# Kernel optimization log

Measured on AMD Instinct MI355X. Metric: run time of the kernel, lower is better.

## Reference

```python
import jax, jax.numpy as jnp
import numpy as np

D = 1024
H = 16
DK = D // H


def setup_inputs() -> dict:
    key = jax.random.key(0)
    ks = jax.random.split(key, 10)
    B, S = 2, 2048
    scale = 1.0 / np.sqrt(D)
    inp = {
        "x": jax.random.normal(ks[0], (B, S, D), dtype=jnp.float32),
        "mask": jax.random.randint(ks[1], (B, S), 0, 2, dtype=jnp.int32),
        "wq": jax.random.normal(ks[2], (D, D), dtype=jnp.float32) * scale,
        "bq": jnp.zeros((D,), dtype=jnp.float32),
        "wk": jax.random.normal(ks[3], (D, D), dtype=jnp.float32) * scale,
        "bk": jnp.zeros((D,), dtype=jnp.float32),
        "wv": jax.random.normal(ks[4], (D, D), dtype=jnp.float32) * scale,
        "bv": jnp.zeros((D,), dtype=jnp.float32),
        "wo": jax.random.normal(ks[5], (D, D), dtype=jnp.float32) * scale,
        "bo": jnp.zeros((D,), dtype=jnp.float32),
    }
    return inp


def reference(x, mask, wq, bq, wk, bk, wv, bv, wo, bo):
    B, S, _ = x.shape
    # torch Linear: y = x @ W.T + b
    def proj(w, b):
        return (jnp.einsum("bsd,ed->bse", x, w) + b).reshape(B, S, H, DK).transpose(0, 2, 1, 3)  # (B,H,S,dk)

    q = proj(wq, bq)
    k = proj(wk, bk)
    v = proj(wv, bv)

    scores = jnp.einsum("bhqd,bhkd->bhqk", q, k) / jnp.sqrt(jnp.float32(DK))  # (B,H,S,S)
    # original: mask.unsqueeze(1).unsqueeze(3) -> (B,1,S,1), masks along the QUERY axis
    m = mask[:, None, :, None]  # (B,1,S,1)
    scores = jnp.where(m == 0, jnp.float32(-1e9), scores)
    attn = jax.nn.softmax(scores, axis=-1)
    ctx = jnp.einsum("bhqk,bhkd->bhqd", attn, v)  # (B,H,S,dk)
    concat = ctx.transpose(0, 2, 1, 3).reshape(B, S, D)
    return jnp.einsum("bsd,ed->bse", concat, wo) + bo
```

## Files before the change

### kernel.cpp

```cpp
#include <hip/hip_runtime.h>
#include <hip/hip_bf16.h>

#define SEQ 2048
#define DM  1024

typedef __attribute__((ext_vector_type(8))) _Float16 f16x8;
typedef __attribute__((ext_vector_type(4)))  float   f32x4;

#define EXP2F(x) __builtin_amdgcn_exp2f(x)

__device__ __forceinline__ ushort f2h(float x) {
    union { _Float16 h; ushort u; } c; c.h = (_Float16)x; return c.u;
}
__device__ __forceinline__ unsigned pk2h(float a, float b) {
    typedef __fp16 fp16v2 __attribute__((ext_vector_type(2)));
    union { fp16v2 h; unsigned u; } c;
    c.h = __builtin_amdgcn_cvt_pkrtz(a, b);
    return c.u;
}

__device__ __forceinline__ void gload16(const void* g, void* l) {
    __builtin_amdgcn_global_load_lds(
        (const __attribute__((address_space(1))) unsigned*)(uintptr_t)g,
        (__attribute__((address_space(3))) unsigned*)(uintptr_t)l, 16, 0, 0);
}

__global__ __launch_bounds__(256)
void cvt_all(const float* __restrict__ x,  const float* __restrict__ wq,
             const float* __restrict__ wk, const float* __restrict__ wv,
             const float* __restrict__ wo,
             ushort* __restrict__ xH, ushort* __restrict__ wH)
{
    const int NX4 = (2 * SEQ * DM) / 4;
    const int NW4 = (DM * DM) / 4;
    const int total = NX4 + 4 * NW4;
    for (int i = blockIdx.x * 256 + threadIdx.x; i < total; i += gridDim.x * 256) {
        float4 v; ushort4* dst;
        if (i < NX4) {
            v = ((const float4*)x)[i];
            dst = (ushort4*)xH + i;
        } else {
            const int j = i - NX4;
            const int wi = j >> 18;
            const int jo = j & (NW4 - 1);
            const float* ws_ = (wi == 0) ? wq : (wi == 1) ? wk : (wi == 2) ? wv : wo;
            v = ((const float4*)ws_)[jo];
            dst = (ushort4*)wH + j;
        }
        ushort4 h;
        h.x = f2h(v.x); h.y = f2h(v.y); h.z = f2h(v.z); h.w = f2h(v.w);
        *dst = h;
    }
}

template<int BM, int BN, int WM, int WN, int MODE>
__global__ __launch_bounds__(WM * WN * 64)
void gemm5(const ushort* __restrict__ A, const ushort* __restrict__ B,
           const float* __restrict__ b0, const float* __restrict__ b1,
           const float* __restrict__ b2,
           ushort* __restrict__ QH, ushort* __restrict__ KH,
           ushort* __restrict__ VH, float* __restrict__ outf, int nmt)
{
    constexpr int NW  = WM * WN;
    constexpr int PR  = BM / WM, PC = BN / WN;
    constexpr int MR  = PR / 16, NR = PC / 16, MH = MR / 2;
    constexpr int APW = (BM / 8) / NW;
    constexpr int BPW = (BN / 8) / NW;
    constexpr int NT  = DM / 64;

    __shared__ ushort A_lds[2][BM * 64];
    __shared__ ushort B_lds[2][BN * 64];

    const int tid = threadIdx.x, w = tid >> 6, lane = tid & 63;
    const int nwg = gridDim.x, q8 = nwg >> 3;
    const int wg  = (blockIdx.x & 7) * q8 + (blockIdx.x >> 3);
    const int m0  = (wg % nmt) * BM, n0 = (wg / nmt) * BN;
    const int wm  = w / WN, wn = w % WN;

    auto stage = [&](int buf, int kt) {
        const int k0 = kt * 64;
#pragma unroll
        for (int j = 0; j < APW; ++j) {
            const int s   = w * APW + j;
            const int row = s * 8 + (lane >> 3);
            const int cl  = (lane & 7) ^ (row & 7);
            gload16(A + (size_t)(m0 + row) * DM + k0 + cl * 8,
                    &A_lds[buf][s * 512]);
        }
#pragma unroll
        for (int j = 0; j < BPW; ++j) {
            const int s   = w * BPW + j;
            const int row = s * 8 + (lane >> 3);
            const int cl  = (lane & 7) ^ (row & 7);
            gload16(B + (size_t)(n0 + row) * DM + k0 + cl * 8,
                    &B_lds[buf][s * 512]);
        }
    };

    f32x4 acc[MR][NR];
#pragma unroll
    for (int i = 0; i < MR; ++i)
#pragma unroll
        for (int j = 0; j < NR; ++j) acc[i][j] = f32x4{0.f, 0.f, 0.f, 0.f};

    stage(0, 0);
    stage(1, 1);

    for (int t = 0; t < NT; ++t) {
        const int buf = t & 1;
        if (t == NT - 1) asm volatile("s_waitcnt vmcnt(0)" ::: "memory");
        else             asm volatile("s_waitcnt vmcnt(8)" ::: "memory");
        __builtin_amdgcn_sched_barrier(0);
        __builtin_amdgcn_s_barrier();

        f16x8 bf_[NR][2];
#pragma unroll
        for (int nf = 0; nf < NR; ++nf) {
            const int r = wn * PC + nf * 16 + (lane & 15);
#pragma unroll
            for (int kb = 0; kb < 2; ++kb) {
                const int c = kb * 4 + (lane >> 4);
                bf_[nf][kb] = *(const f16x8*)&B_lds[buf][r * 64 + ((c ^ (r & 7)) << 3)];
            }
        }
#pragma unroll
        for (int qm = 0; qm < 2; ++qm) {
            f16x8 af_[MH][2];
#pragma unroll
            for (int mf = 0; mf < MH; ++mf) {
                const int r = wm * PR + qm * (PR / 2) + mf * 16 + (lane & 15);
#pragma unroll
                for (int kb = 0; kb < 2; ++kb) {
                    const int c = kb * 4 + (lane >> 4);
                    af_[mf][kb] = *(const f16x8*)&A_lds[buf][r * 64 + ((c ^ (r & 7)) << 3)];
                }
            }
            __builtin_amdgcn_s_setprio(1);
#pragma unroll
            for (int kb = 0; kb < 2; ++kb)
#pragma unroll
                for (int mf = 0; mf < MH; ++mf)
#pragma unroll
                    for (int nf = 0; nf < NR; ++nf)
                        acc[qm * MH + mf][nf] = __builtin_amdgcn_mfma_f32_16x16x32_f16(
                            af_[mf][kb], bf_[nf][kb], acc[qm * MH + mf][nf], 0, 0, 0);
            __builtin_amdgcn_s_setprio(0);
        }
        __builtin_amdgcn_sched_barrier(0);
        __builtin_amdgcn_s_barrier();
        __builtin_amdgcn_sched_barrier(0);
        if (t + 2 < NT) stage(buf, t + 2);
    }

#pragma unroll
    for (int mf = 0; mf < MR; ++mf)
#pragma unroll
        for (int nf = 0; nf < NR; ++nf) {
            const int col  = n0 + wn * PC + nf * 16 + (lane & 15);
            const int row0 = m0 + wm * PR + mf * 16 + ((lane >> 4) << 2);
            f32x4 v = acc[mf][nf];
            if constexpr (MODE == 1) {
                float4 o;
                o.x = v[0] + b0[row0 + 0];
                o.y = v[1] + b0[row0 + 1];
                o.z = v[2] + b0[row0 + 2];
                o.w = v[3] + b0[row0 + 3];
                *(float4*)&outf[(size_t)col * DM + row0] = o;
            } else {
                const int sel = row0 >> 10;
                const int e = row0 & 1023;
                const int b = col >> 11, s = col & 2047;
                const int h = e >> 6, dk = e & 63;
                const float* bp = (sel == 0) ? b0 : (sel == 1) ? b1 : b2;
                const float sc = (sel == 0) ? 0.125f * 1.44269504089f : 1.0f;
                const float v0 = (v[0] + bp[e + 0]) * sc;
                const float v1 = (v[1] + bp[e + 1]) * sc;
                const float v2 = (v[2] + bp[e + 2]) * sc;
                const float v3 = (v[3] + bp[e + 3]) * sc;
                const int bh = b * 16 + h;
                ushort4 hv;
                hv.x = f2h(v0); hv.y = f2h(v1); hv.z = f2h(v2); hv.w = f2h(v3);
                if (sel == 0) {
                    const size_t off = ((size_t)bh * SEQ + s) * 64 + dk;
                    *(ushort4*)&QH[off] = hv;
                } else if (sel == 1) {
                    const size_t off = ((size_t)bh * SEQ + s) * 64 + dk;
                    *(ushort4*)&KH[off] = hv;
                } else {
                    const size_t o0 = ((size_t)bh * 64 + dk) * SEQ + s;
                    VH[o0]           = hv.x;
                    VH[o0 + SEQ]     = hv.y;
                    VH[o0 + 2 * SEQ] = hv.z;
                    VH[o0 + 3 * SEQ] = hv.w;
                }
            }
        }
}

__global__ __launch_bounds__(512, 2)
void attn_k(const ushort* __restrict__ QH, const ushort* __restrict__ KH,
            const ushort* __restrict__ VH, const int* __restrict__ mask,
            ushort* __restrict__ ch)
{
    __shared__ ushort Ks[2][64 * 64];
    __shared__ ushort Vs[2][64 * 64];
    __shared__ ushort Ps[8][16 * 64];

    const int t = threadIdx.x, w = t >> 6, lane = t & 63;
    const int wg = (blockIdx.x & 7) * 64 + (blockIdx.x >> 3);
    const int bh = wg >> 4, qt = wg & 15;
    const int b = bh >> 4, h = bh & 15;
    const int q0 = qt * 128 + w * 16;
    const size_t base = (size_t)bh * SEQ * 64;
    const int lq = lane & 15, cb = lane >> 4;

    const int msk = mask[b * SEQ + q0 + lq];
    f16x8 qf[2];
#pragma unroll
    for (int kb = 0; kb < 2; ++kb) {
        qf[kb] = *(const f16x8*)&QH[base + (size_t)(q0 + lq) * 64 + kb * 32 + cb * 8];
        if (msk == 0) qf[kb] = f16x8{0, 0, 0, 0, 0, 0, 0, 0};
    }

    float m_run = -1e30f, l_run = 0.f;
    f32x4 acc[4];
#pragma unroll
    for (int df = 0; df < 4; ++df) acc[df] = f32x4{0.f, 0.f, 0.f, 0.f};

    f16x8 sK, sV;
    const int sr = t >> 3, scc = t & 7;
    const int wr_off = sr * 64 + (scc ^ (sr & 7)) * 8;
    const f16x8* pK = (const f16x8*)&KH[base + (size_t)sr * 64 + scc * 8];
    const ushort* gK = &KH[base + (size_t)sr * 64 + scc * 8];
    const ushort* gV = &VH[base + (size_t)sr * SEQ + scc * 8];
    auto stage_load = [&]() {
        sK = *(const f16x8*)gK;
        sV = *(const f16x8*)gV;
        gK += 64 * 64;
        gV += 64;
    };

    stage_load();
    *(f16x8*)&Ks[0][wr_off] = sK;
    *(f16x8*)&Vs[0][wr_off] = sV;
    stage_load();
    __syncthreads();

    auto body = [&](const int BUF, const bool WR, const bool LD) {
        if (WR) {
            *(f16x8*)&Ks[BUF ^ 1][wr_off] = sK;
            *(f16x8*)&Vs[BUF ^ 1][wr_off] = sV;
        }
        if (LD) stage_load();

        f32x4 st[4];
#pragma unroll
        for (int mf = 0; mf < 4; ++mf) st[mf] = f32x4{0.f, 0.f, 0.f, 0.f};
        __builtin_amdgcn_s_setprio(1);
#pragma unroll
        for (int mf = 0; mf < 4; ++mf) {
            const int r = mf * 16 + lq;
#pragma unroll
            for (int kb = 0; kb < 2; ++kb) {
                const int p = (kb * 4 + cb) ^ (r & 7);
                f16x8 kf = *(const f16x8*)&Ks[BUF][r * 64 + p * 8];
                st[mf] = __builtin_amdgcn_mfma_f32_16x16x32_f16(kf, qf[kb], st[mf], 0, 0, 0);
            }
        }
        __builtin_amdgcn_s_setprio(0);

        {
            float mx = -1e30f;
#pragma unroll
            for (int mf = 0; mf < 4; ++mf)
#pragma unroll
                for (int r4 = 0; r4 < 4; ++r4) mx = fmaxf(mx, st[mf][r4]);
            if (!__all(mx - m_run <= 8.0f)) {
                mx = fmaxf(mx, __shfl_xor(mx, 16));
                mx = fmaxf(mx, __shfl_xor(mx, 32));
                const float mnew = fmaxf(m_run, mx);
                const float corr = EXP2F(m_run - mnew);
                m_run = mnew;
                l_run *= corr;
#pragma unroll
                for (int df = 0; df < 4; ++df)
#pragma unroll
                    for (int r4 = 0; r4 < 4; ++r4) acc[df][r4] *= corr;
            }
            float ss = 0.f;
#pragma unroll
            for (int mf = 0; mf < 4; ++mf)
#pragma unroll
                for (int r4 = 0; r4 < 4; ++r4) {
                    const float p = EXP2F(st[mf][r4] - m_run);
                    st[mf][r4] = p; ss += p;
                }
            ss += __shfl_xor(ss, 16);
            ss += __shfl_xor(ss, 32);
            l_run += ss;
        }

#pragma unroll
        for (int mf = 0; mf < 4; ++mf) {
            const int key0 = mf * 16 + (cb << 2);
            uint2 pw;
            pw.x = pk2h(st[mf][0], st[mf][1]);
            pw.y = pk2h(st[mf][2], st[mf][3]);
            const int p = (key0 >> 3) ^ (lq & 7);
            *(uint2*)&Ps[w][lq * 64 + p * 8 + (key0 & 7)] = pw;
        }

        f16x8 pf[2];
#pragma unroll
        for (int kb = 0; kb < 2; ++kb) {
            const int p = (kb * 4 + cb) ^ (lq & 7);
            pf[kb] = *(const f16x8*)&Ps[w][lq * 64 + p * 8];
        }
        __builtin_amdgcn_s_setprio(1);
#pragma unroll
        for (int df = 0; df < 4; ++df) {
            const int r = df * 16 + lq;
#pragma unroll
            for (int kb = 0; kb < 2; ++kb) {
                const int p = (kb * 4 + cb) ^ (r & 7);
                f16x8 vf = *(const f16x8*)&Vs[BUF][r * 64 + p * 8];
                acc[df] = __builtin_amdgcn_mfma_f32_16x16x32_f16(vf, pf[kb], acc[df], 0, 0, 0);
            }
        }
        __builtin_amdgcn_s_setprio(0);

        __syncthreads();
    };

#pragma unroll 1
    for (int i = 0; i < 15; ++i) {
        body(0, true, true);
        body(1, true, true);
    }
    body(0, true, false);
    body(1, false, false);

    {
        const float inv = 1.0f / l_run;
        const int s = q0 + lq;
#pragma unroll
        for (int df = 0; df < 4; ++df) {
            const int e0 = h * 64 + df * 16 + (cb << 2);
            ushort4 hv;
            hv.x = f2h(acc[df][0] * inv);
            hv.y = f2h(acc[df][1] * inv);
            hv.z = f2h(acc[df][2] * inv);
            hv.w = f2h(acc[df][3] * inv);
            *(ushort4*)&ch[(size_t)(b * SEQ + s) * DM + e0] = hv;
        }
    }
}

extern "C" void kernel_launch(void* const* d_in, const int* in_sizes, int n_in,
                              void* d_out, int out_size, void* d_ws, size_t ws_size,
                              hipStream_t stream)
{
    const float* x  = (const float*)d_in[0];
    const int* mask = (const int*)d_in[1];
    const float* wq = (const float*)d_in[2];
    const float* bq = (const float*)d_in[3];
    const float* wk = (const float*)d_in[4];
    const float* bk = (const float*)d_in[5];
    const float* wv = (const float*)d_in[6];
    const float* bv = (const float*)d_in[7];
    const float* wo = (const float*)d_in[8];
    const float* bo = (const float*)d_in[9];
    float* out = (float*)d_out;

    const size_t M1 = 1024 * 1024;
    ushort* W = (ushort*)d_ws;
    ushort* xH = W;
    ushort* wH = W + 4 * M1;
    ushort* QH = W + 8 * M1;
    ushort* KH = W + 12 * M1;
    ushort* VH = W + 16 * M1;

    cvt_all<<<2048, 256, 0, stream>>>(x, wq, wk, wv, wo, xH, wH);

    gemm5<384, 128, 4, 2, 0><<<256, 512, 0, stream>>>(
        wH, xH, bq, bk, bv, QH, KH, VH, nullptr, 8);

    attn_k<<<512, 512, 0, stream>>>(QH, KH, VH, mask, xH);

    gemm5<128, 128, 2, 2, 1><<<256, 256, 0, stream>>>(
        wH + 3 * M1, xH, bo, nullptr, nullptr,
        nullptr, nullptr, nullptr, out, 8);
}
```

Baseline: 109.9 us.

## Software-pipeline QK^T of the next tile with softmax/PV of the previous tile

Moves the attention kernel to a triple-buffered K/V shared-memory ring. The QK^T MFMAs for tile i+1 are issued before the softmax and PV MFMAs for tile i, so the exp and scalar softmax work can overlap matrix-core work. This costs 8 more score registers per thread and more LDS, which risks spills or lower occupancy. The prefetch also reads one tile past the end of each head.

After: 107.7 us. No clear change (-2.0%).

```diff
diff --git a/kernel.cpp b/kernel.cpp
--- a/kernel.cpp
+++ b/kernel.cpp
@@ -202,8 +202,8 @@
             const ushort* __restrict__ VH, const int* __restrict__ mask,
             ushort* __restrict__ ch)
 {
-    __shared__ ushort Ks[2][64 * 64];
-    __shared__ ushort Vs[2][64 * 64];
+    __shared__ ushort K3[3][64 * 64];
+    __shared__ ushort V3[3][64 * 64];
     __shared__ ushort Ps[8][16 * 64];
 
     const int t = threadIdx.x, w = t >> 6, lane = t & 63;
@@ -227,118 +227,132 @@
 #pragma unroll
     for (int df = 0; df < 4; ++df) acc[df] = f32x4{0.f, 0.f, 0.f, 0.f};
 
+    f32x4 stb[2][4];
+
     f16x8 sK, sV;
     const int sr = t >> 3, scc = t & 7;
     const int wr_off = sr * 64 + (scc ^ (sr & 7)) * 8;
-    const f16x8* pK = (const f16x8*)&KH[base + (size_t)sr * 64 + scc * 8];
     const ushort* gK = &KH[base + (size_t)sr * 64 + scc * 8];
     const ushort* gV = &VH[base + (size_t)sr * SEQ + scc * 8];
-    auto stage_load = [&]() {
-        sK = *(const f16x8*)gK;
-        sV = *(const f16x8*)gV;
-        gK += 64 * 64;
-        gV += 64;
-    };
-
-    stage_load();
-    *(f16x8*)&Ks[0][wr_off] = sK;
-    *(f16x8*)&Vs[0][wr_off] = sV;
-    stage_load();
+
+    sK = *(const f16x8*)gK; sV = *(const f16x8*)gV; gK += 4096; gV += 64;
+    *(f16x8*)&K3[0][wr_off] = sK; *(f16x8*)&V3[0][wr_off] = sV;
+    sK = *(const f16x8*)gK; sV = *(const f16x8*)gV; gK += 4096; gV += 64;
+    *(f16x8*)&K3[1][wr_off] = sK; *(f16x8*)&V3[1][wr_off] = sV;
+    sK = *(const f16x8*)gK; sV = *(const f16x8*)gV; gK += 4096; gV += 64;
     __syncthreads();
 
-    auto body = [&](const int BUF, const bool WR, const bool LD) {
-        if (WR) {
-            *(f16x8*)&Ks[BUF ^ 1][wr_off] = sK;
-            *(f16x8*)&Vs[BUF ^ 1][wr_off] = sV;
-        }
-        if (LD) stage_load();
-
-        f32x4 st[4];
-#pragma unroll
-        for (int mf = 0; mf < 4; ++mf) st[mf] = f32x4{0.f, 0.f, 0.f, 0.f};
-        __builtin_amdgcn_s_setprio(1);
-#pragma unroll
-        for (int mf = 0; mf < 4; ++mf) {
-            const int r = mf * 16 + lq;
-#pragma unroll
-            for (int kb = 0; kb < 2; ++kb) {
-                const int p = (kb * 4 + cb) ^ (r & 7);
-                f16x8 kf = *(const f16x8*)&Ks[BUF][r * 64 + p * 8];
-                st[mf] = __builtin_amdgcn_mfma_f32_16x16x32_f16(kf, qf[kb], st[mf], 0, 0, 0);
-            }
-        }
-        __builtin_amdgcn_s_setprio(0);
-
-        {
-            float mx = -1e30f;
-#pragma unroll
-            for (int mf = 0; mf < 4; ++mf)
-#pragma unroll
-                for (int r4 = 0; r4 < 4; ++r4) mx = fmaxf(mx, st[mf][r4]);
-            if (!__all(mx - m_run <= 8.0f)) {
-                mx = fmaxf(mx, __shfl_xor(mx, 16));
-                mx = fmaxf(mx, __shfl_xor(mx, 32));
-                const float mnew = fmaxf(m_run, mx);
-                const float corr = EXP2F(m_run - mnew);
-                m_run = mnew;
-                l_run *= corr;
-#pragma unroll
-                for (int df = 0; df < 4; ++df)
-#pragma unroll
-                    for (int r4 = 0; r4 < 4; ++r4) acc[df][r4] *= corr;
-            }
-            float ss = 0.f;
-#pragma unroll
-            for (int mf = 0; mf < 4; ++mf)
-#pragma unroll
-                for (int r4 = 0; r4 < 4; ++r4) {
-                    const float p = EXP2F(st[mf][r4] - m_run);
-                    st[mf][r4] = p; ss += p;
-                }
-            ss += __shfl_xor(ss, 16);
-            ss += __shfl_xor(ss, 32);
-            l_run += ss;
-        }
-
-#pragma unroll
-        for (int mf = 0; mf < 4; ++mf) {
-            const int key0 = mf * 16 + (cb << 2);
-            uint2 pw;
-            pw.x = pk2h(st[mf][0], st[mf][1]);
-            pw.y = pk2h(st[mf][2], st[mf][3]);
-            const int p = (key0 >> 3) ^ (lq & 7);
-            *(uint2*)&Ps[w][lq * 64 + p * 8 + (key0 & 7)] = pw;
-        }
-
-        f16x8 pf[2];
-#pragma unroll
-        for (int kb = 0; kb < 2; ++kb) {
-            const int p = (kb * 4 + cb) ^ (lq & 7);
-            pf[kb] = *(const f16x8*)&Ps[w][lq * 64 + p * 8];
-        }
-        __builtin_amdgcn_s_setprio(1);
-#pragma unroll
-        for (int df = 0; df < 4; ++df) {
-            const int r = df * 16 + lq;
-#pragma unroll
-            for (int kb = 0; kb < 2; ++kb) {
-                const int p = (kb * 4 + cb) ^ (r & 7);
-                f16x8 vf = *(const f16x8*)&Vs[BUF][r * 64 + p * 8];
-                acc[df] = __builtin_amdgcn_mfma_f32_16x16x32_f16(vf, pf[kb], acc[df], 0, 0, 0);
-            }
-        }
-        __builtin_amdgcn_s_setprio(0);
-
-        __syncthreads();
-    };
+#define QKM(B3, CUR)                                                          \
+    {                                                                         \
+        _Pragma("unroll")                                                     \
+        for (int mf = 0; mf < 4; ++mf) stb[CUR][mf] = f32x4{0.f,0.f,0.f,0.f}; \
+        __builtin_amdgcn_s_setprio(1);                                        \
+        _Pragma("unroll")                                                     \
+        for (int mf = 0; mf < 4; ++mf) {                                      \
+            const int r_ = mf * 16 + lq;                                      \
+            _Pragma("unroll")                                                 \
+            for (int kb = 0; kb < 2; ++kb) {                                  \
+                const int p_ = (kb * 4 + cb) ^ (r_ & 7);                      \
+                f16x8 kf = *(const f16x8*)&K3[B3][r_ * 64 + p_ * 8];          \
+                stb[CUR][mf] = __builtin_amdgcn_mfma_f32_16x16x32_f16(        \
+                    kf, qf[kb], stb[CUR][mf], 0, 0, 0);                       \
+            }                                                                 \
+        }                                                                     \
+        __builtin_amdgcn_s_setprio(0);                                        \
+    }
+
+#define FINP(PRV, VB)                                                         \
+    {                                                                         \
+        float ma = fmaxf(fmaxf(stb[PRV][0][0], stb[PRV][0][1]),               \
+                         fmaxf(stb[PRV][0][2], stb[PRV][0][3]));              \
+        float mb = fmaxf(fmaxf(stb[PRV][1][0], stb[PRV][1][1]),               \
+                         fmaxf(stb[PRV][1][2], stb[PRV][1][3]));              \
+        float mc = fmaxf(fmaxf(stb[PRV][2][0], stb[PRV][2][1]),               \
+                         fmaxf(stb[PRV][2][2], stb[PRV][2][3]));              \
+        float md = fmaxf(fmaxf(stb[PRV][3][0], stb[PRV][3][1]),               \
+                         fmaxf(stb[PRV][3][2], stb[PRV][3][3]));              \
+        float mx = fmaxf(fmaxf(ma, mb), fmaxf(mc, md));                       \
+        if (!__all(mx - m_run <= 8.0f)) {                                     \
+            mx = fmaxf(mx, __shfl_xor(mx, 16));                               \
+            mx = fmaxf(mx, __shfl_xor(mx, 32));                               \
+            const float mnew = fmaxf(m_run, mx);                              \
+            const float corr = EXP2F(m_run - mnew);                           \
+            m_run = mnew;                                                     \
+            l_run *= corr;                                                    \
+            _Pragma("unroll")                                                 \
+            for (int df = 0; df < 4; ++df)                                    \
+                _Pragma("unroll")                                             \
+                for (int r4 = 0; r4 < 4; ++r4) acc[df][r4] *= corr;           \
+        }                                                                     \
+        float parts[4];                                                       \
+        _Pragma("unroll")                                                     \
+        for (int mf = 0; mf < 4; ++mf) {                                      \
+            float e0 = EXP2F(stb[PRV][mf][0] - m_run);                        \
+            float e1 = EXP2F(stb[PRV][mf][1] - m_run);                        \
+            float e2 = EXP2F(stb[PRV][mf][2] - m_run);                        \
+            float e3 = EXP2F(stb[PRV][mf][3] - m_run);                        \
+            parts[mf] = (e0 + e1) + (e2 + e3);                                \
+            uint2 pw;                                                         \
+            pw.x = pk2h(e0, e1);                                              \
+            pw.y = pk2h(e2, e3);                                              \
+            const int key0 = mf * 16 + (cb << 2);                             \
+            const int p_ = (key0 >> 3) ^ (lq & 7);                            \
+            *(uint2*)&Ps[w][lq * 64 + p_ * 8 + (key0 & 7)] = pw;              \
+        }                                                                     \
+        float ss = (parts[0] + parts[1]) + (parts[2] + parts[3]);             \
+        ss += __shfl_xor(ss, 16);                                             \
+        ss += __shfl_xor(ss, 32);                                             \
+        l_run += ss;                                                          \
+        f16x8 pf[2];                                                          \
+        _Pragma("unroll")                                                     \
+        for (int kb = 0; kb < 2; ++kb) {                                      \
+            const int p_ = (kb * 4 + cb) ^ (lq & 7);                          \
+            pf[kb] = *(const f16x8*)&Ps[w][lq * 64 + p_ * 8];                 \
+        }                                                                     \
+        __builtin_amdgcn_s_setprio(1);                                        \
+        _Pragma("unroll")                                                     \
+        for (int df = 0; df < 4; ++df) {                                      \
+            const int r_ = df * 16 + lq;                                      \
+            _Pragma("unroll")                                                 \
+            for (int kb = 0; kb < 2; ++kb) {                                  \
+                const int p_ = (kb * 4 + cb) ^ (r_ & 7);                      \
+                f16x8 vf = *(const f16x8*)&V3[VB][r_ * 64 + p_ * 8];          \
+                acc[df] = __builtin_amdgcn_mfma_f32_16x16x32_f16(             \
+                    vf, pf[kb], acc[df], 0, 0, 0);                            \
+            }                                                                 \
+        }                                                                     \
+        __builtin_amdgcn_s_setprio(0);                                        \
+    }
+
+#define STEP(B3, WB, VB, CUR, PRV)                                            \
+    {                                                                         \
+        QKM(B3, CUR);                                                         \
+        *(f16x8*)&K3[WB][wr_off] = sK;                                        \
+        *(f16x8*)&V3[WB][wr_off] = sV;                                        \
+        sK = *(const f16x8*)gK;                                               \
+        sV = *(const f16x8*)gV;                                               \
+        gK += 4096; gV += 64;                                                 \
+        FINP(PRV, VB);                                                        \
+        __syncthreads();                                                      \
+    }
+
+    QKM(0, 0);
 
 #pragma unroll 1
-    for (int i = 0; i < 15; ++i) {
-        body(0, true, true);
-        body(1, true, true);
-    }
-    body(0, true, false);
-    body(1, false, false);
+    for (int i = 0; i < 5; ++i) {
+        STEP(1, 2, 0, 1, 0);
+        STEP(2, 0, 1, 0, 1);
+        STEP(0, 1, 2, 1, 0);
+        STEP(1, 2, 0, 0, 1);
+        STEP(2, 0, 1, 1, 0);
+        STEP(0, 1, 2, 0, 1);
+    }
+    STEP(1, 2, 0, 1, 0);
+    FINP(1, 1);
+
+#undef STEP
+#undef FINP
+#undef QKM
 
     {
         const float inv = 1.0f / l_run;
```
